# Performance work log

Hardware: AMD Instinct MI355X
Metric: run time of the kernel (lower is better)

## Reference

```python
import jax, jax.numpy as jnp
import numpy as np

ROPE_BASE = 10000.0


def rotate_half(x):
    # interleaved rotate: (x0,x1,x2,x3,...) -> (-x1,x0,-x3,x2,...)
    x1 = x[..., ::2]
    x2 = x[..., 1::2]
    return jnp.stack((-x2, x1), axis=-1).reshape(x.shape)


def rope_cos_sin(seq_len, dim, dtype):
    inv_freq = 1.0 / (ROPE_BASE ** (jnp.arange(0, dim, 2, dtype=jnp.float32) / dim))
    pos = jnp.arange(seq_len, dtype=jnp.float32)
    freqs = jnp.outer(pos, inv_freq)              # [S, dim/2]
    emb = jnp.concatenate([freqs, freqs], axis=-1)  # [S, dim]
    return jnp.cos(emb).astype(dtype), jnp.sin(emb).astype(dtype)


def setup_inputs() -> dict:
    key = jax.random.key(0)
    k1, k2, k3, k4 = jax.random.split(key, 4)
    B, S, D = 4, 4096, 256
    scale = 1.0 / np.sqrt(D)
    x = jax.random.normal(k1, (B, S, D), dtype=jnp.float32)
    wq = jax.random.normal(k2, (D, D), dtype=jnp.float32) * scale
    wk = jax.random.normal(k3, (D, D), dtype=jnp.float32) * scale
    wv = jax.random.normal(k4, (D, D), dtype=jnp.float32) * scale
    return {"x": x, "wq": wq, "wk": wk, "wv": wv}


def reference(x, wq, wk, wv):
    D = x.shape[-1]
    S = x.shape[-2]
    # torch Linear: y = x @ W^T
    q = jnp.einsum('bsd,ed->bse', x, wq)
    k = jnp.einsum('bsd,ed->bse', x, wk)
    v = jnp.einsum('bsd,ed->bse', x, wv)
    cos, sin = rope_cos_sin(S, D, x.dtype)  # [S, D]
    q = q * cos + rotate_half(q) * sin
    k = k * cos + rotate_half(k) * sin
    scores = jnp.einsum('bqd,bkd->bqk', q, k) / jnp.sqrt(jnp.asarray(D, x.dtype))
    weights = jax.nn.softmax(scores, axis=-1)
    output = jnp.einsum('bqk,bkd->bqd', weights, v)
    return output, weights
```

## Files before the change

kernel.cpp:

```cpp
#include <hip/hip_runtime.h>
#include <hip/hip_bf16.h>
#include <stdint.h>


#define B_ 4
#define S_ 4096
#define D_ 256
#define NQ 4194304
#define NW 65536
#define NTAB 524288

typedef __attribute__((ext_vector_type(4))) float f32x4;
typedef __attribute__((ext_vector_type(8))) short short8;
typedef __attribute__((ext_vector_type(4))) short short4v;
typedef __attribute__((ext_vector_type(4))) unsigned uint32x4;

__device__ __forceinline__ short f2bf(float f) {
  unsigned u = __builtin_bit_cast(unsigned, f);
  u += 0x7fffu + ((u >> 16) & 1u);
  return (short)(u >> 16);
}
__device__ __forceinline__ float bf2f(short h) {
  unsigned u = ((unsigned)(unsigned short)h) << 16;
  return __builtin_bit_cast(float, u);
}

__device__ __forceinline__ void gload16(const void* g, void* l) {
  __builtin_amdgcn_global_load_lds(
      (const __attribute__((address_space(1))) unsigned*)g,
      (__attribute__((address_space(3))) unsigned*)l, 16, 0, 0);
}

__global__ __launch_bounds__(256) void k0_split(
    const float* __restrict__ x, const float* __restrict__ wq,
    const float* __restrict__ wk, const float* __restrict__ wv,
    short* __restrict__ xh, short* __restrict__ xl,
    short* __restrict__ wh, short* __restrict__ wl,
    float* __restrict__ ctab) {
  int idx = blockIdx.x * 256 + threadIdx.x;
  if (idx < NQ) {
    float v = x[idx];
    short hi = f2bf(v);
    xh[idx] = hi;
    xl[idx] = f2bf(v - bf2f(hi));
  } else if (idx < NQ + 3 * NW) {
    int r = idx - NQ;
    int m = r >> 16;
    int e = r & (NW - 1);
    const float* w = (m == 0) ? wq : (m == 1) ? wk : wv;
    float v = w[e];
    short hi = f2bf(v);
    wh[r] = hi;
    wl[r] = f2bf(v - bf2f(hi));
  } else {
    int t = idx - NQ - 3 * NW;
    int s = t >> 7, j = t & 127;
    float invf = __expf(-0.07195578415606394f * (float)j);
    float sn, cs;
    sincosf((float)s * invf, &sn, &cs);
    ctab[2 * t] = cs;
    ctab[2 * t + 1] = sn;
  }
}

__global__ __launch_bounds__(256) void k1_proj(
    const short* __restrict__ xh, const short* __restrict__ xl,
    const short* __restrict__ wh, const short* __restrict__ wl,
    const float* __restrict__ ctab,
    short* __restrict__ qh, short* __restrict__ ql,
    short* __restrict__ kh, short* __restrict__ vt) {
  const int m = blockIdx.y;
  const int b = blockIdx.x >> 6;
  const int sbase = (blockIdx.x & 63) << 6;
  const int tid = threadIdx.x;
  const int w = tid >> 6;
  const int lane = tid & 63;
  const int lr = lane & 15;
  const int g = lane >> 4;

  const int srow = sbase + w * 16 + lr;
  const short* xhp = xh + ((size_t)(b * S_ + srow)) * D_;
  const short* xlp = xl + ((size_t)(b * S_ + srow)) * D_;
  const short* whm = wh + m * NW;
  const short* wlm = wl + m * NW;

  f32x4 acc[16];
#pragma unroll
  for (int i = 0; i < 16; ++i) acc[i] = (f32x4)0.f;

#pragma unroll
  for (int dc = 0; dc < 8; ++dc) {
    const int d = dc * 32 + g * 8;
    short8 ah = *(const short8*)(xhp + d);
    short8 al = *(const short8*)(xlp + d);
#pragma unroll
    for (int ct = 0; ct < 16; ++ct) {
      const int e = ct * 16 + lr;
      short8 bh = *(const short8*)(whm + e * D_ + d);
      short8 bl = *(const short8*)(wlm + e * D_ + d);
      acc[ct] = __builtin_amdgcn_mfma_f32_16x16x32_bf16(ah, bh, acc[ct], 0, 0, 0);
      acc[ct] = __builtin_amdgcn_mfma_f32_16x16x32_bf16(ah, bl, acc[ct], 0, 0, 0);
      acc[ct] = __builtin_amdgcn_mfma_f32_16x16x32_bf16(al, bh, acc[ct], 0, 0, 0);
    }
  }

  const int s0 = sbase + w * 16 + g * 4;
  if (m == 2) {
#pragma unroll
    for (int ct = 0; ct < 16; ++ct) {
      const int e = ct * 16 + lr;
      short4v pk;
#pragma unroll
      for (int r = 0; r < 4; ++r) pk[r] = f2bf(acc[ct][r]);
      *(short4v*)(vt + ((size_t)(b * D_ + e)) * S_ + s0) = pk;
    }
  } else {
    short* oh = (m == 0) ? qh : kh;
#pragma unroll
    for (int ct = 0; ct < 16; ++ct) {
      const int e = ct * 16 + lr;
      const float sgn = (e & 1) ? 1.0f : -1.0f;
#pragma unroll
      for (int r = 0; r < 4; ++r) {
        float v = acc[ct][r];
        float p = __shfl_xor(v, 1, 64);
        const float2 cs2 = *(const float2*)(ctab + ((size_t)((s0 + r) << 7) + (e & 127)) * 2);
        float q2 = v * cs2.x + sgn * p * cs2.y;
        short hi = f2bf(q2);
        size_t off = ((size_t)(b * S_ + s0 + r)) * D_ + e;
        oh[off] = hi;
        if (m == 0) ql[off] = f2bf(q2 - bf2f(hi));
      }
    }
  }
}

__global__ __launch_bounds__(256, 2) void k2_fused(
    const short* __restrict__ qh, const short* __restrict__ ql,
    const short* __restrict__ kh, const short* __restrict__ vt,
    float* __restrict__ wts, float* __restrict__ out) {
  __shared__ __align__(16) char kbuf[32768];
  __shared__ __align__(16) char etile[2][2048];
  __shared__ float part[2][32];
  __shared__ float lsum_l[32];

  const int bid = blockIdx.x;
  const int swz = (bid & 7) * 64 + ((bid >> 3) & 31) * 2 + (bid >> 8);
  const int b = swz >> 7;
  const int qbase = (swz & 127) << 5;
  const int tid = threadIdx.x;
  const int w = tid >> 6;
  const int lane = tid & 63;
  const int lr = lane & 15;
  const int g = lane >> 4;
  const int qg = w & 1;
  const int kg = w >> 1;

  short8 qfh[8], qfl[8];
  {
    const int qrow = qbase + qg * 16 + lr;
    const short* ph = qh + ((size_t)(b * S_ + qrow)) * D_;
    const short* pl = ql + ((size_t)(b * S_ + qrow)) * D_;
#pragma unroll
    for (int dc = 0; dc < 8; ++dc) {
      qfh[dc] = *(const short8*)(ph + dc * 32 + g * 8);
      qfl[dc] = *(const short8*)(pl + dc * 32 + g * 8);
    }
  }

  f32x4 acc = (f32x4)0.f;
  f32x4 accv[2][4];
#pragma unroll
  for (int qs = 0; qs < 2; ++qs)
#pragma unroll
    for (int dt = 0; dt < 4; ++dt) accv[qs][dt] = (f32x4)0.f;
  float rs = 0.f;

  const char* khb = (const char*)(kh + (size_t)b * S_ * D_);
  const short* vtb = vt + (size_t)b * D_ * S_;
  const int swx = (lane & 7) << 4;

  float* WBf = wts + ((size_t)(b * S_ + qbase)) * S_;

  auto STAGE = [&](int kt, char* dst) {
#pragma unroll
    for (int i = 0; i < 4; ++i) {
      const int p = i * 4096 + tid * 16;
      const int xo = p ^ (((p >> 9) & 7) << 4);
      gload16(khb + (size_t)kt * 16384 + xo, dst + p);
    }
  };

  STAGE(0, kbuf);
  __syncthreads();

  for (int kt = 0; kt < 128; ++kt) {
    const int cur = kt & 1;
    const char* kb = kbuf + cur * 16384;

    if (kt < 127) STAGE(kt + 1, kbuf + (cur ^ 1) * 16384);

    if (kt > 0) {
      const char* et = etile[cur ^ 1];
      __builtin_amdgcn_s_setprio(1);
      short8 ea0 = *(const short8*)(et + ((lr * 64 + g * 16) ^ ((lr & 3) << 4)));
      short8 ea1 = *(const short8*)(et + (((16 + lr) * 64 + g * 16) ^ ((lr & 3) << 4)));
#pragma unroll
      for (int dt = 0; dt < 4; ++dt) {
        const int d = w * 64 + dt * 16 + lr;
        short8 vb = *(const short8*)(vtb + (size_t)d * S_ + (kt - 1) * 32 + g * 8);
        accv[0][dt] = __builtin_amdgcn_mfma_f32_16x16x32_bf16(ea0, vb, accv[0][dt], 0, 0, 0);
        accv[1][dt] = __builtin_amdgcn_mfma_f32_16x16x32_bf16(ea1, vb, accv[1][dt], 0, 0, 0);
      }
      __builtin_amdgcn_s_setprio(0);
    }

    __builtin_amdgcn_s_setprio(1);
#pragma unroll
    for (int dc = 0; dc < 8; ++dc) {
      const int row = kg * 16 + lr;
      const int x = (row * 512 + dc * 64 + g * 16) ^ swx;
      short8 afh = *(const short8*)(kb + x);
      acc = __builtin_amdgcn_mfma_f32_16x16x32_bf16(afh, qfh[dc], acc, 0, 0, 0);
      acc = __builtin_amdgcn_mfma_f32_16x16x32_bf16(afh, qfl[dc], acc, 0, 0, 0);
    }
    __builtin_amdgcn_s_setprio(0);

    {
      f32x4 e;
#pragma unroll
      for (int r = 0; r < 4; ++r) e[r] = __expf(acc[r] * 0.0625f);
      rs += e[0] + e[1] + e[2] + e[3];
      unsigned lo = (unsigned)(unsigned short)f2bf(e[0]) |
                    ((unsigned)(unsigned short)f2bf(e[1]) << 16);
      unsigned hi2 = (unsigned)(unsigned short)f2bf(e[2]) |
                     ((unsigned)(unsigned short)f2bf(e[3]) << 16);
      const int row = qg * 16 + lr;
      const int colb = (kg * 16 + g * 4) * 2;
      const int ad = (row * 64 + colb) ^ ((row & 3) << 4);
      *(uint2*)(etile[cur] + ad) = make_uint2(lo, hi2);
      acc = (f32x4)0.f;
    }
    __syncthreads();
  }

  {
    const char* et = etile[1];
    short8 ea0 = *(const short8*)(et + ((lr * 64 + g * 16) ^ ((lr & 3) << 4)));
    short8 ea1 = *(const short8*)(et + (((16 + lr) * 64 + g * 16) ^ ((lr & 3) << 4)));
#pragma unroll
    for (int dt = 0; dt < 4; ++dt) {
      const int d = w * 64 + dt * 16 + lr;
      short8 vb = *(const short8*)(vtb + (size_t)d * S_ + 127 * 32 + g * 8);
      accv[0][dt] = __builtin_amdgcn_mfma_f32_16x16x32_bf16(ea0, vb, accv[0][dt], 0, 0, 0);
      accv[1][dt] = __builtin_amdgcn_mfma_f32_16x16x32_bf16(ea1, vb, accv[1][dt], 0, 0, 0);
    }
  }

  rs += __shfl_xor(rs, 16, 64);
  rs += __shfl_xor(rs, 32, 64);
  if (lane < 16) part[kg][qg * 16 + lane] = rs;
  __syncthreads();
  if (tid < 32) lsum_l[tid] = part[0][tid] + part[1][tid];
  __syncthreads();

  {
    float* ob = out + (size_t)b * S_ * D_;
    float rv[2][4];
#pragma unroll
    for (int qs = 0; qs < 2; ++qs)
#pragma unroll
      for (int r = 0; r < 4; ++r)
        rv[qs][r] = 1.0f / lsum_l[qs * 16 + g * 4 + r];
#pragma unroll
    for (int qs = 0; qs < 2; ++qs)
#pragma unroll
      for (int dt = 0; dt < 4; ++dt)
#pragma unroll
        for (int r = 0; r < 4; ++r) {
          const int q = qbase + qs * 16 + g * 4 + r;
          ob[(size_t)q * D_ + w * 64 + dt * 16 + lr] = accv[qs][dt][r] * rv[qs][r];
        }
  }

  const float rinvw = 1.0f / lsum_l[qg * 16 + lr];
  float* wrow = WBf + (size_t)(qg * 16 + lr) * S_ + kg * 16 + g * 4;

  STAGE(0, kbuf);
  __syncthreads();

  for (int kt = 0; kt < 128; ++kt) {
    const int cur = kt & 1;
    const char* kb = kbuf + cur * 16384;

    if (kt < 127) STAGE(kt + 1, kbuf + (cur ^ 1) * 16384);

    f32x4 a2 = (f32x4)0.f;
    __builtin_amdgcn_s_setprio(1);
#pragma unroll
    for (int dc = 0; dc < 8; ++dc) {
      const int row = kg * 16 + lr;
      const int x = (row * 512 + dc * 64 + g * 16) ^ swx;
      short8 afh = *(const short8*)(kb + x);
      a2 = __builtin_amdgcn_mfma_f32_16x16x32_bf16(afh, qfh[dc], a2, 0, 0, 0);
      a2 = __builtin_amdgcn_mfma_f32_16x16x32_bf16(afh, qfl[dc], a2, 0, 0, 0);
    }
    __builtin_amdgcn_s_setprio(0);

    f32x4 wv;
#pragma unroll
    for (int r = 0; r < 4; ++r) wv[r] = __expf(a2[r] * 0.0625f) * rinvw;
    *(f32x4*)(wrow + kt * 32) = wv;

    __syncthreads();
  }
}

extern "C" void kernel_launch(void* const* d_in, const int* in_sizes, int n_in,
                              void* d_out, int out_size, void* d_ws, size_t ws_size,
                              hipStream_t stream) {
  const float* x  = (const float*)d_in[0];
  const float* wq = (const float*)d_in[1];
  const float* wk = (const float*)d_in[2];
  const float* wv = (const float*)d_in[3];

  float* out = (float*)d_out;
  float* wts = out + (size_t)B_ * S_ * D_;

  short* xh = (short*)d_ws;
  short* xl = xh + NQ;
  short* qh = xl + NQ;
  short* ql = qh + NQ;
  short* kh = ql + NQ;
  short* vt = kh + NQ;
  short* wh = vt + NQ;
  short* wl = wh + 3 * NW;
  float* ctab = (float*)(wl + 3 * NW);

  k0_split<<<dim3((NQ + 3 * NW + NTAB) / 256), 256, 0, stream>>>(
      x, wq, wk, wv, xh, xl, wh, wl, ctab);
  k1_proj<<<dim3(B_ * S_ / 64, 3), 256, 0, stream>>>(
      xh, xl, wh, wl, ctab, qh, ql, kh, vt);
  k2_fused<<<dim3(512), 256, 0, stream>>>(
      qh, ql, kh, vt, wts, out);
}
```

Measured before the change: 473.0 us.

## Split keys across wave halves and drop LDS staging of K tiles

Each wave now owns half of the key sequence for its 16 query rows and reads K and V fragments straight from global memory, with no shared-memory double buffering and no per-iteration block barriers. Each wave keeps a private exp tile in shared memory and accumulates the full 256-wide output. The two halves are merged through a shared-memory output buffer at the end. This removes the __syncthreads per tile and the async LDS copies. In exchange it uses 16 accumulator vectors per wave, which raises register pressure, and every wave re-reads K directly from global memory or cache instead of sharing one staged copy.

After: 835.9 us. 1.77x slower.

```diff
diff --git a/kernel.cpp b/kernel.cpp
--- a/kernel.cpp
+++ b/kernel.cpp
@@ -13,7 +13,6 @@
 typedef __attribute__((ext_vector_type(4))) float f32x4;
 typedef __attribute__((ext_vector_type(8))) short short8;
 typedef __attribute__((ext_vector_type(4))) short short4v;
-typedef __attribute__((ext_vector_type(4))) unsigned uint32x4;
 
 __device__ __forceinline__ short f2bf(float f) {
   unsigned u = __builtin_bit_cast(unsigned, f);
@@ -23,12 +22,6 @@
 __device__ __forceinline__ float bf2f(short h) {
   unsigned u = ((unsigned)(unsigned short)h) << 16;
   return __builtin_bit_cast(float, u);
-}
-
-__device__ __forceinline__ void gload16(const void* g, void* l) {
-  __builtin_amdgcn_global_load_lds(
-      (const __attribute__((address_space(1))) unsigned*)g,
-      (__attribute__((address_space(3))) unsigned*)l, 16, 0, 0);
 }
 
 __global__ __launch_bounds__(256) void k0_split(
@@ -139,8 +132,8 @@
     const short* __restrict__ qh, const short* __restrict__ ql,
     const short* __restrict__ kh, const short* __restrict__ vt,
     float* __restrict__ wts, float* __restrict__ out) {
-  __shared__ __align__(16) char kbuf[32768];
-  __shared__ __align__(16) char etile[2][2048];
+  __shared__ __align__(16) char etile[4][2048];
+  __shared__ float obuf[2][16][256];
   __shared__ float part[2][32];
   __shared__ float lsum_l[32];
 
@@ -154,7 +147,7 @@
   const int lr = lane & 15;
   const int g = lane >> 4;
   const int qg = w & 1;
-  const int kg = w >> 1;
+  const int khalf = w >> 1;
 
   short8 qfh[8], qfl[8];
   {
@@ -168,151 +161,109 @@
     }
   }
 
-  f32x4 acc = (f32x4)0.f;
-  f32x4 accv[2][4];
-#pragma unroll
-  for (int qs = 0; qs < 2; ++qs)
-#pragma unroll
-    for (int dt = 0; dt < 4; ++dt) accv[qs][dt] = (f32x4)0.f;
+  f32x4 accv[16];
+#pragma unroll
+  for (int i = 0; i < 16; ++i) accv[i] = (f32x4)0.f;
   float rs = 0.f;
 
-  const char* khb = (const char*)(kh + (size_t)b * S_ * D_);
+  const short* kbase = kh + ((size_t)b * S_ + khalf * 2048) * D_;
   const short* vtb = vt + (size_t)b * D_ * S_;
-  const int swx = (lane & 7) << 4;
+  char* et = etile[w];
+  const int wsw = (lr & 7) << 4;
 
   float* WBf = wts + ((size_t)(b * S_ + qbase)) * S_;
 
-  auto STAGE = [&](int kt, char* dst) {
-#pragma unroll
-    for (int i = 0; i < 4; ++i) {
-      const int p = i * 4096 + tid * 16;
-      const int xo = p ^ (((p >> 9) & 7) << 4);
-      gload16(khb + (size_t)kt * 16384 + xo, dst + p);
-    }
-  };
-
-  STAGE(0, kbuf);
-  __syncthreads();
-
-  for (int kt = 0; kt < 128; ++kt) {
-    const int cur = kt & 1;
-    const char* kb = kbuf + cur * 16384;
-
-    if (kt < 127) STAGE(kt + 1, kbuf + (cur ^ 1) * 16384);
-
-    if (kt > 0) {
-      const char* et = etile[cur ^ 1];
-      __builtin_amdgcn_s_setprio(1);
-      short8 ea0 = *(const short8*)(et + ((lr * 64 + g * 16) ^ ((lr & 3) << 4)));
-      short8 ea1 = *(const short8*)(et + (((16 + lr) * 64 + g * 16) ^ ((lr & 3) << 4)));
-#pragma unroll
-      for (int dt = 0; dt < 4; ++dt) {
-        const int d = w * 64 + dt * 16 + lr;
-        short8 vb = *(const short8*)(vtb + (size_t)d * S_ + (kt - 1) * 32 + g * 8);
-        accv[0][dt] = __builtin_amdgcn_mfma_f32_16x16x32_bf16(ea0, vb, accv[0][dt], 0, 0, 0);
-        accv[1][dt] = __builtin_amdgcn_mfma_f32_16x16x32_bf16(ea1, vb, accv[1][dt], 0, 0, 0);
+  for (int kt = 0; kt < 64; ++kt) {
+    const short* krow = kbase + (size_t)kt * 32 * D_;
+
+    f32x4 acc0 = (f32x4)0.f, acc1 = (f32x4)0.f;
+#pragma unroll
+    for (int dc = 0; dc < 8; ++dc) {
+      short8 a0 = *(const short8*)(krow + lr * D_ + dc * 32 + g * 8);
+      short8 a1 = *(const short8*)(krow + (16 + lr) * D_ + dc * 32 + g * 8);
+      acc0 = __builtin_amdgcn_mfma_f32_16x16x32_bf16(a0, qfh[dc], acc0, 0, 0, 0);
+      acc0 = __builtin_amdgcn_mfma_f32_16x16x32_bf16(a0, qfl[dc], acc0, 0, 0, 0);
+      acc1 = __builtin_amdgcn_mfma_f32_16x16x32_bf16(a1, qfh[dc], acc1, 0, 0, 0);
+      acc1 = __builtin_amdgcn_mfma_f32_16x16x32_bf16(a1, qfl[dc], acc1, 0, 0, 0);
+    }
+
+    {
+      f32x4 e0, e1;
+#pragma unroll
+      for (int r = 0; r < 4; ++r) {
+        e0[r] = __expf(acc0[r] * 0.0625f);
+        e1[r] = __expf(acc1[r] * 0.0625f);
       }
-      __builtin_amdgcn_s_setprio(0);
-    }
-
-    __builtin_amdgcn_s_setprio(1);
-#pragma unroll
-    for (int dc = 0; dc < 8; ++dc) {
-      const int row = kg * 16 + lr;
-      const int x = (row * 512 + dc * 64 + g * 16) ^ swx;
-      short8 afh = *(const short8*)(kb + x);
-      acc = __builtin_amdgcn_mfma_f32_16x16x32_bf16(afh, qfh[dc], acc, 0, 0, 0);
-      acc = __builtin_amdgcn_mfma_f32_16x16x32_bf16(afh, qfl[dc], acc, 0, 0, 0);
-    }
-    __builtin_amdgcn_s_setprio(0);
-
-    {
-      f32x4 e;
-#pragma unroll
-      for (int r = 0; r < 4; ++r) e[r] = __expf(acc[r] * 0.0625f);
-      rs += e[0] + e[1] + e[2] + e[3];
-      unsigned lo = (unsigned)(unsigned short)f2bf(e[0]) |
-                    ((unsigned)(unsigned short)f2bf(e[1]) << 16);
-      unsigned hi2 = (unsigned)(unsigned short)f2bf(e[2]) |
-                     ((unsigned)(unsigned short)f2bf(e[3]) << 16);
-      const int row = qg * 16 + lr;
-      const int colb = (kg * 16 + g * 4) * 2;
-      const int ad = (row * 64 + colb) ^ ((row & 3) << 4);
-      *(uint2*)(etile[cur] + ad) = make_uint2(lo, hi2);
-      acc = (f32x4)0.f;
-    }
-    __syncthreads();
-  }
-
-  {
-    const char* et = etile[1];
-    short8 ea0 = *(const short8*)(et + ((lr * 64 + g * 16) ^ ((lr & 3) << 4)));
-    short8 ea1 = *(const short8*)(et + (((16 + lr) * 64 + g * 16) ^ ((lr & 3) << 4)));
-#pragma unroll
-    for (int dt = 0; dt < 4; ++dt) {
-      const int d = w * 64 + dt * 16 + lr;
-      short8 vb = *(const short8*)(vtb + (size_t)d * S_ + 127 * 32 + g * 8);
-      accv[0][dt] = __builtin_amdgcn_mfma_f32_16x16x32_bf16(ea0, vb, accv[0][dt], 0, 0, 0);
-      accv[1][dt] = __builtin_amdgcn_mfma_f32_16x16x32_bf16(ea1, vb, accv[1][dt], 0, 0, 0);
+      rs += e0[0] + e0[1] + e0[2] + e0[3] + e1[0] + e1[1] + e1[2] + e1[3];
+      uint2 p0, p1;
+      p0.x = (unsigned)(unsigned short)f2bf(e0[0]) | ((unsigned)(unsigned short)f2bf(e0[1]) << 16);
+      p0.y = (unsigned)(unsigned short)f2bf(e0[2]) | ((unsigned)(unsigned short)f2bf(e0[3]) << 16);
+      p1.x = (unsigned)(unsigned short)f2bf(e1[0]) | ((unsigned)(unsigned short)f2bf(e1[1]) << 16);
+      p1.y = (unsigned)(unsigned short)f2bf(e1[2]) | ((unsigned)(unsigned short)f2bf(e1[3]) << 16);
+      *(uint2*)(et + ((lr * 128 + 0 * 32 + g * 8) ^ wsw)) = p0;
+      *(uint2*)(et + ((lr * 128 + 1 * 32 + g * 8) ^ wsw)) = p1;
+    }
+    short8 ea = *(const short8*)(et + ((lr * 128 + g * 16) ^ wsw));
+#pragma unroll
+    for (int dt = 0; dt < 16; ++dt) {
+      short8 vb = *(const short8*)(vtb + (size_t)(dt * 16 + lr) * S_ +
+                                   khalf * 2048 + kt * 32 + g * 8);
+      accv[dt] = __builtin_amdgcn_mfma_f32_16x16x32_bf16(ea, vb, accv[dt], 0, 0, 0);
     }
   }
 
   rs += __shfl_xor(rs, 16, 64);
   rs += __shfl_xor(rs, 32, 64);
-  if (lane < 16) part[kg][qg * 16 + lane] = rs;
+  if (lane < 16) part[khalf][qg * 16 + lane] = rs;
+  if (khalf == 1) {
+#pragma unroll
+    for (int dt = 0; dt < 16; ++dt)
+#pragma unroll
+      for (int r = 0; r < 4; ++r)
+        obuf[qg][4 * g + r][dt * 16 + lr] = accv[dt][r];
+  }
   __syncthreads();
   if (tid < 32) lsum_l[tid] = part[0][tid] + part[1][tid];
   __syncthreads();
 
-  {
+  if (khalf == 0) {
     float* ob = out + (size_t)b * S_ * D_;
-    float rv[2][4];
-#pragma unroll
-    for (int qs = 0; qs < 2; ++qs)
-#pragma unroll
-      for (int r = 0; r < 4; ++r)
-        rv[qs][r] = 1.0f / lsum_l[qs * 16 + g * 4 + r];
-#pragma unroll
-    for (int qs = 0; qs < 2; ++qs)
-#pragma unroll
-      for (int dt = 0; dt < 4; ++dt)
-#pragma unroll
-        for (int r = 0; r < 4; ++r) {
-          const int q = qbase + qs * 16 + g * 4 + r;
-          ob[(size_t)q * D_ + w * 64 + dt * 16 + lr] = accv[qs][dt][r] * rv[qs][r];
-        }
+    float rv[4];
+#pragma unroll
+    for (int r = 0; r < 4; ++r) rv[r] = 1.0f / lsum_l[qg * 16 + 4 * g + r];
+#pragma unroll
+    for (int dt = 0; dt < 16; ++dt)
+#pragma unroll
+      for (int r = 0; r < 4; ++r) {
+        const int q = qbase + qg * 16 + 4 * g + r;
+        ob[(size_t)q * D_ + dt * 16 + lr] =
+            (accv[dt][r] + obuf[qg][4 * g + r][dt * 16 + lr]) * rv[r];
+      }
   }
 
   const float rinvw = 1.0f / lsum_l[qg * 16 + lr];
-  float* wrow = WBf + (size_t)(qg * 16 + lr) * S_ + kg * 16 + g * 4;
-
-  STAGE(0, kbuf);
-  __syncthreads();
-
-  for (int kt = 0; kt < 128; ++kt) {
-    const int cur = kt & 1;
-    const char* kb = kbuf + cur * 16384;
-
-    if (kt < 127) STAGE(kt + 1, kbuf + (cur ^ 1) * 16384);
-
-    f32x4 a2 = (f32x4)0.f;
-    __builtin_amdgcn_s_setprio(1);
+  float* wrow = WBf + (size_t)(qg * 16 + lr) * S_ + khalf * 2048;
+
+  for (int kt = 0; kt < 64; ++kt) {
+    const short* krow = kbase + (size_t)kt * 32 * D_;
+    f32x4 acc0 = (f32x4)0.f, acc1 = (f32x4)0.f;
 #pragma unroll
     for (int dc = 0; dc < 8; ++dc) {
-      const int row = kg * 16 + lr;
-      const int x = (row * 512 + dc * 64 + g * 16) ^ swx;
-      short8 afh = *(const short8*)(kb + x);
-      a2 = __builtin_amdgcn_mfma_f32_16x16x32_bf16(afh, qfh[dc], a2, 0, 0, 0);
-      a2 = __builtin_amdgcn_mfma_f32_16x16x32_bf16(afh, qfl[dc], a2, 0, 0, 0);
-    }
-    __builtin_amdgcn_s_setprio(0);
-
-    f32x4 wv;
-#pragma unroll
-    for (int r = 0; r < 4; ++r) wv[r] = __expf(a2[r] * 0.0625f) * rinvw;
-    *(f32x4*)(wrow + kt * 32) = wv;
-
-    __syncthreads();
+      short8 a0 = *(const short8*)(krow + lr * D_ + dc * 32 + g * 8);
+      short8 a1 = *(const short8*)(krow + (16 + lr) * D_ + dc * 32 + g * 8);
+      acc0 = __builtin_amdgcn_mfma_f32_16x16x32_bf16(a0, qfh[dc], acc0, 0, 0, 0);
+      acc0 = __builtin_amdgcn_mfma_f32_16x16x32_bf16(a0, qfl[dc], acc0, 0, 0, 0);
+      acc1 = __builtin_amdgcn_mfma_f32_16x16x32_bf16(a1, qfh[dc], acc1, 0, 0, 0);
+      acc1 = __builtin_amdgcn_mfma_f32_16x16x32_bf16(a1, qfl[dc], acc1, 0, 0, 0);
+    }
+    f32x4 w0, w1;
+#pragma unroll
+    for (int r = 0; r < 4; ++r) {
+      w0[r] = __expf(acc0[r] * 0.0625f) * rinvw;
+      w1[r] = __expf(acc1[r] * 0.0625f) * rinvw;
+    }
+    *(f32x4*)(wrow + kt * 32 + 4 * g) = w0;
+    *(f32x4*)(wrow + kt * 32 + 16 + 4 * g) = w1;
   }
 }
 
```
